# Kernel optimization log

Measured on AMD Instinct MI355X. Metric: run time of the kernel, lower is better.

## Reference

```python
import jax, jax.numpy as jnp
import numpy as np

# Vim-S config
B, L, D, DEPTH = 16, 197, 384, 24
DI, DS, DTR = 768, 16, 24  # d_inner=2*D, d_state, dt_rank=ceil(D/16)
NUM_CLASSES = 1000
EPS = 1e-5


def setup_inputs() -> dict:
    key = jax.random.key(0)
    ks = jax.random.split(key, 12)
    f = jnp.float32
    rn = lambda k, shp, s=0.02: jax.random.normal(k, shp, f) * s
    inp = {
        'x': jax.random.normal(ks[0], (B, 3, 224, 224), f),
        'patch_w': rn(ks[1], (D, 3, 16, 16)),
        'patch_b': jnp.zeros((D,), f),
        'cls_token': rn(ks[2], (1, 1, D)),
        'pos_embed': rn(ks[3], (1, L, D)),
        'in_proj_w': rn(ks[4], (DEPTH, 2 * DI, D)),
        'conv_w': rn(ks[5], (DEPTH, DI, 1, 4), 0.1),  # depthwise causal conv, d_conv=4
        'conv_b': jnp.zeros((DEPTH, DI), f),
        'x_proj_w': rn(ks[6], (DEPTH, DTR + 2 * DS, DI)),
        'dt_proj_w': rn(ks[7], (DEPTH, DI, DTR), 0.1),
        'dt_proj_b': jnp.full((DEPTH, DI), float(np.log(np.expm1(0.01))), f),
        'A_log': jnp.log(jnp.broadcast_to(jnp.arange(1, DS + 1, dtype=f), (DEPTH, DI, DS))),
        'D_ssm': jnp.ones((DEPTH, DI), f),
        'out_proj_w': rn(ks[8], (DEPTH, D, DI)),
        'norm_w': jnp.ones((DEPTH, D), f),
        'norm_b': jnp.zeros((DEPTH, D), f),
        'normf_w': jnp.ones((D,), f),
        'normf_b': jnp.zeros((D,), f),
        'head_w': rn(ks[9], (NUM_CLASSES, D)),
        'head_b': jnp.zeros((NUM_CLASSES,), f),
    }
    return inp


def _ln(u, w, b):
    mu = u.mean(-1, keepdims=True)
    v = ((u - mu) ** 2).mean(-1, keepdims=True)
    return (u - mu) * jax.lax.rsqrt(v + EPS) * w + b


def _silu(u):
    return u * jax.nn.sigmoid(u)


def _mixer(u, Win, Wc, bc, Wx, Wdt, bdt, Alog, Dp, Wout):
    # u: [B, L, D]
    xz = jnp.einsum('bld,ed->ble', u, Win)            # [B, L, 2*DI]
    xc, z = jnp.split(xz, 2, axis=-1)
    # causal depthwise conv1d (d_conv=4): pad 3 on the left
    xt = jnp.pad(xc.transpose(0, 2, 1), ((0, 0), (0, 0), (3, 0)))
    xt = jax.lax.conv_general_dilated(xt, Wc, (1,), 'VALID',
                                      dimension_numbers=('NCH', 'OIH', 'NCH'),
                                      feature_group_count=DI)
    xc = _silu((xt + bc[None, :, None]).transpose(0, 2, 1))  # [B, L, DI]
    dbl = jnp.einsum('bld,ed->ble', xc, Wx)           # [B, L, DTR+2*DS]
    dt = jax.nn.softplus(jnp.einsum('blr,dr->bld', dbl[..., :DTR], Wdt) + bdt)
    Bm = dbl[..., DTR:DTR + DS]                       # [B, L, DS]
    Cm = dbl[..., DTR + DS:]                          # [B, L, DS]
    A = -jnp.exp(Alog)                                # [DI, DS]
    dA = jnp.exp(jnp.einsum('bld,dn->bldn', dt, A))   # [B, L, DI, DS]
    dBx = jnp.einsum('bld,bln->bldn', dt * xc, Bm)    # [B, L, DI, DS]

    def step(h, inps):
        dA_t, dBx_t, C_t = inps
        h = dA_t * h + dBx_t                          # [B, DI, DS]
        return h, jnp.einsum('bdn,bn->bd', h, C_t)

    h0 = jnp.zeros((u.shape[0], DI, DS), u.dtype)
    _, ys = jax.lax.scan(step, h0, (dA.transpose(1, 0, 2, 3),
                                    dBx.transpose(1, 0, 2, 3),
                                    Cm.transpose(1, 0, 2)))
    y = ys.transpose(1, 0, 2) + xc * Dp               # [B, L, DI]
    y = y * _silu(z)
    return jnp.einsum('ble,de->bld', y, Wout)         # [B, L, D]


def reference(x, patch_w, patch_b, cls_token, pos_embed, in_proj_w, conv_w, conv_b,
              x_proj_w, dt_proj_w, dt_proj_b, A_log, D_ssm, out_proj_w,
              norm_w, norm_b, normf_w, normf_b, head_w, head_b):
    b = x.shape[0]
    # patch embed: Conv2d(3, D, 16, stride 16)
    feat = jax.lax.conv_general_dilated(x, patch_w, (16, 16), 'VALID',
                                        dimension_numbers=('NCHW', 'OIHW', 'NCHW'))
    feat = feat + patch_b[None, :, None, None]
    tokens = feat.reshape(b, D, -1).transpose(0, 2, 1)          # [B, 196, D]
    h = jnp.concatenate([jnp.broadcast_to(cls_token, (b, 1, D)), tokens], axis=1)
    h = h + pos_embed                                           # [B, 197, D]

    def layer(carry, p):
        hid, res = carry
        Win, Wc, bc, Wx, Wdt, bdt, Alog, Dp, Wout, nw, nb = p
        res = res + hid                # (hidden + residual), first layer: residual = hidden
        hid = _mixer(_ln(res, nw, nb), Win, Wc, bc, Wx, Wdt, bdt, Alog, Dp, Wout)
        return (hid, res), None

    (hid, res), _ = jax.lax.scan(layer, (h, jnp.zeros_like(h)),
                                 (in_proj_w, conv_w, conv_b, x_proj_w, dt_proj_w,
                                  dt_proj_b, A_log, D_ssm, out_proj_w, norm_w, norm_b))
    out = _ln(res + hid, normf_w, normf_b)
    return out[:, 0] @ head_w.T + head_b                        # [B, num_classes]
```

## Files before the change

kernel.cpp:

```cpp
#include <hip/hip_runtime.h>
#include <hip/hip_bf16.h>
#include <math.h>

#define BB     16
#define LL     197
#define DD     384
#define DEPTH  24
#define DI     768
#define DSN    16
#define DTR    24
#define NC     1000
#define TT     (BB*LL)
#define NPATCH 196
#define EPSV   1e-5f

#define NCHUNK 12
#define CH     17

typedef __attribute__((ext_vector_type(8))) short short8;
typedef __attribute__((ext_vector_type(4))) short short4v;
typedef __attribute__((ext_vector_type(4))) float f32x4;

__device__ __forceinline__ short f2bf(float f) {
  union { float f; unsigned u; } v; v.f = f;
  unsigned u = v.u + 0x7fffu + ((v.u >> 16) & 1u);
  return (short)(u >> 16);
}

__device__ __forceinline__ void gload16(const short* g, const short* l) {
  __builtin_amdgcn_global_load_lds(
      (const __attribute__((address_space(1))) unsigned int*)g,
      (__attribute__((address_space(3))) unsigned int*)l, 16, 0, 0);
}

__global__ __launch_bounds__(256) void k_cvt(const float* __restrict__ src,
                                             short* __restrict__ dst, int n) {
  int i = (blockIdx.x * 256 + threadIdx.x) * 4;
  if (i + 3 < n) {
    float4 v = *(const float4*)&src[i];
    short4v o = {f2bf(v.x), f2bf(v.y), f2bf(v.z), f2bf(v.w)};
    *(short4v*)&dst[i] = o;
  } else {
    for (int j = 0; i + j < n && j < 4; j++) dst[i + j] = f2bf(src[i + j]);
  }
}

__global__ __launch_bounds__(256) void k_init(const float* __restrict__ cls,
                                              const float* __restrict__ pos,
                                              float* __restrict__ res,
                                              float* __restrict__ hid) {
  int i = blockIdx.x * 256 + threadIdx.x;
  if (i < TT * DD) res[i] = 0.f;
  if (i < BB * DD) {
    int b = i / DD, d = i % DD;
    hid[(size_t)(b * LL) * DD + d] = cls[d] + pos[d];
  }
}

__global__ __launch_bounds__(256) void k_patch(const float* __restrict__ x,
                                               const float* __restrict__ pw,
                                               const float* __restrict__ pb,
                                               const float* __restrict__ pos,
                                               float* __restrict__ hid) {
  __shared__ short sA[64 * 40];
  __shared__ short sB[64 * 40];
  const int tid = threadIdx.x;
  const int m0 = blockIdx.x * 64, n0 = blockIdx.y * 64;
  const int srow = tid >> 2;
  const int skq = (tid & 3) * 8;
  const int lane = tid & 63, w = tid >> 6;
  const int wm = (w >> 1) * 32, wn = (w & 1) * 32;
  const int fr = lane & 15;
  const int fk = (lane >> 4) * 8;
  f32x4 acc[2][2] = {};
  const int m = m0 + srow;
  const int b = m / NPATCH;
  const int p = m % NPATCH;
  const int ph = p / 14, pwi = p % 14;
  const float* Wrow = pw + (size_t)(n0 + srow) * 768 + skq;
  for (int k0 = 0; k0 < 768; k0 += 32) {
    int k = k0 + skq;
    int c = k >> 8, rr = (k >> 4) & 15, kw = k & 15;
    const float* xrow = &x[(size_t)(((b * 3 + c) * 224) + (ph * 16 + rr)) * 224 +
                           (pwi * 16 + kw)];
    float4 a0 = *(const float4*)&xrow[0];
    float4 a1 = *(const float4*)&xrow[4];
    float4 b0 = *(const float4*)&Wrow[k0];
    float4 b1 = *(const float4*)&Wrow[k0 + 4];
    short8 av = {f2bf(a0.x), f2bf(a0.y), f2bf(a0.z), f2bf(a0.w),
                 f2bf(a1.x), f2bf(a1.y), f2bf(a1.z), f2bf(a1.w)};
    short8 bv = {f2bf(b0.x), f2bf(b0.y), f2bf(b0.z), f2bf(b0.w),
                 f2bf(b1.x), f2bf(b1.y), f2bf(b1.z), f2bf(b1.w)};
    *(short8*)&sA[srow * 40 + skq] = av;
    *(short8*)&sB[srow * 40 + skq] = bv;
    __syncthreads();
    short8 af0 = *(const short8*)&sA[(wm + fr) * 40 + fk];
    short8 af1 = *(const short8*)&sA[(wm + 16 + fr) * 40 + fk];
    short8 bf0 = *(const short8*)&sB[(wn + fr) * 40 + fk];
    short8 bf1 = *(const short8*)&sB[(wn + 16 + fr) * 40 + fk];
    acc[0][0] = __builtin_amdgcn_mfma_f32_16x16x32_bf16(af0, bf0, acc[0][0], 0, 0, 0);
    acc[0][1] = __builtin_amdgcn_mfma_f32_16x16x32_bf16(af0, bf1, acc[0][1], 0, 0, 0);
    acc[1][0] = __builtin_amdgcn_mfma_f32_16x16x32_bf16(af1, bf0, acc[1][0], 0, 0, 0);
    acc[1][1] = __builtin_amdgcn_mfma_f32_16x16x32_bf16(af1, bf1, acc[1][1], 0, 0, 0);
    __syncthreads();
  }
#pragma unroll
  for (int i = 0; i < 2; i++)
#pragma unroll
    for (int j = 0; j < 2; j++)
#pragma unroll
      for (int q = 0; q < 4; q++) {
        int mm = m0 + wm + i * 16 + (lane >> 4) * 4 + q;
        int nn = n0 + wn + j * 16 + (lane & 15);
        int b2 = mm / NPATCH, pp = mm % NPATCH;
        int tok = b2 * LL + 1 + pp;
        hid[(size_t)tok * DD + nn] = acc[i][j][q] + pb[nn] + pos[(size_t)(1 + pp) * DD + nn];
      }
}

__global__ __launch_bounds__(256) void k_gemm128(const short* __restrict__ A, int lda,
                                                 const short* __restrict__ W, int ldb,
                                                 float* __restrict__ C, int ldc,
                                                 int M, int N, int K) {
  __shared__ short sA[128 * 32];
  __shared__ short sB[128 * 32];
  const int tid = threadIdx.x;
  const int lane = tid & 63, w = tid >> 6;
  const int m0 = blockIdx.x * 128, n0 = blockIdx.y * 128;
  const int wm = (w >> 1) * 64, wn = (w & 1) * 64;
  const int fr = lane & 15;
  const int fk = (lane >> 4) * 8;
  const int q0 = w * 2, q1 = w * 2 + 1;
  const int sr0 = q0 * 16 + (lane >> 2);
  const int sr1 = q1 * 16 + (lane >> 2);
  const int scol = (lane & 3) * 8;
  f32x4 acc[4][4] = {};
  const short* Ab0 = A + (size_t)(m0 + sr0) * lda + scol;
  const short* Ab1 = A + (size_t)(m0 + sr1) * lda + scol;
  const short* Bb0 = W + (size_t)(n0 + sr0) * ldb + scol;
  const short* Bb1 = W + (size_t)(n0 + sr1) * ldb + scol;
  for (int k0 = 0; k0 < K; k0 += 32) {
    gload16(Ab0 + k0, &sA[q0 * 512]);
    gload16(Ab1 + k0, &sA[q1 * 512]);
    gload16(Bb0 + k0, &sB[q0 * 512]);
    gload16(Bb1 + k0, &sB[q1 * 512]);
    __syncthreads();
    short8 af[4], bf[4];
#pragma unroll
    for (int i = 0; i < 4; i++) {
      af[i] = *(const short8*)&sA[(wm + i * 16 + fr) * 32 + fk];
      bf[i] = *(const short8*)&sB[(wn + i * 16 + fr) * 32 + fk];
    }
#pragma unroll
    for (int i = 0; i < 4; i++)
#pragma unroll
      for (int j = 0; j < 4; j++)
        acc[i][j] = __builtin_amdgcn_mfma_f32_16x16x32_bf16(af[i], bf[j], acc[i][j], 0, 0, 0);
    __syncthreads();
  }
#pragma unroll
  for (int i = 0; i < 4; i++)
#pragma unroll
    for (int j = 0; j < 4; j++)
#pragma unroll
      for (int q = 0; q < 4; q++) {
        int mm = m0 + wm + i * 16 + (lane >> 4) * 4 + q;
        int nn = n0 + wn + j * 16 + fr;
        if (mm < M) C[(size_t)mm * ldc + nn] = acc[i][j][q];
      }
}

__global__ __launch_bounds__(256) void k_gemm64(const short* __restrict__ A, int lda,
                                                const short* __restrict__ W, int ldb,
                                                float* __restrict__ C, int ldc,
                                                int M, int N, int K) {
  __shared__ short sA[64 * 32];
  __shared__ short sB[64 * 32];
  const int tid = threadIdx.x;
  const int lane = tid & 63, w = tid >> 6;
  const int m0 = blockIdx.x * 64, n0 = blockIdx.y * 64;
  const int wm = (w >> 1) * 32, wn = (w & 1) * 32;
  const int fr = lane & 15;
  const int fk = (lane >> 4) * 8;
  const int srow = w * 16 + (lane >> 2);
  const int scol = (lane & 3) * 8;
  f32x4 acc[2][2] = {};
  const short* Ab = A + (size_t)(m0 + srow) * lda + scol;
  const short* Bb = W + (size_t)(n0 + srow) * ldb + scol;
  for (int k0 = 0; k0 < K; k0 += 32) {
    gload16(Ab + k0, &sA[w * 512]);
    gload16(Bb + k0, &sB[w * 512]);
    __syncthreads();
    short8 af0 = *(const short8*)&sA[(wm + fr) * 32 + fk];
    short8 af1 = *(const short8*)&sA[(wm + 16 + fr) * 32 + fk];
    short8 bf0 = *(const short8*)&sB[(wn + fr) * 32 + fk];
    short8 bf1 = *(const short8*)&sB[(wn + 16 + fr) * 32 + fk];
    acc[0][0] = __builtin_amdgcn_mfma_f32_16x16x32_bf16(af0, bf0, acc[0][0], 0, 0, 0);
    acc[0][1] = __builtin_amdgcn_mfma_f32_16x16x32_bf16(af0, bf1, acc[0][1], 0, 0, 0);
    acc[1][0] = __builtin_amdgcn_mfma_f32_16x16x32_bf16(af1, bf0, acc[1][0], 0, 0, 0);
    acc[1][1] = __builtin_amdgcn_mfma_f32_16x16x32_bf16(af1, bf1, acc[1][1], 0, 0, 0);
    __syncthreads();
  }
#pragma unroll
  for (int i = 0; i < 2; i++)
#pragma unroll
    for (int j = 0; j < 2; j++)
#pragma unroll
      for (int q = 0; q < 4; q++) {
        int mm = m0 + wm + i * 16 + (lane >> 4) * 4 + q;
        int nn = n0 + wn + j * 16 + fr;
        if (mm < M) C[(size_t)mm * ldc + nn] = acc[i][j][q];
      }
}

__global__ __launch_bounds__(256) void k_dtproj(const float* __restrict__ A,
                                                const short* __restrict__ W,
                                                const float* __restrict__ bias,
                                                float* __restrict__ C) {
  __shared__ short sA[64 * 40];
  __shared__ short sB[64 * 40];
  const int tid = threadIdx.x;
  const int m0 = blockIdx.x * 64, n0 = blockIdx.y * 64;
  const int srow = tid >> 2;
  const int skq = (tid & 3) * 8;
  const int lane = tid & 63, w = tid >> 6;
  const int wm = (w >> 1) * 32, wn = (w & 1) * 32;
  const int fr = lane & 15;
  const int fk = (lane >> 4) * 8;
  f32x4 acc[2][2] = {};
  const int am = m0 + srow;
  short8 av = {0, 0, 0, 0, 0, 0, 0, 0}, bv = {0, 0, 0, 0, 0, 0, 0, 0};
  if (skq < 24) {
    if (am < TT) {
      float4 a0 = *(const float4*)&A[(size_t)am * 56 + skq];
      float4 a1 = *(const float4*)&A[(size_t)am * 56 + skq + 4];
      av = short8{f2bf(a0.x), f2bf(a0.y), f2bf(a0.z), f2bf(a0.w),
                  f2bf(a1.x), f2bf(a1.y), f2bf(a1.z), f2bf(a1.w)};
    }
    bv = *(const short8*)&W[(size_t)(n0 + srow) * 24 + skq];
  }
  *(short8*)&sA[srow * 40 + skq] = av;
  *(short8*)&sB[srow * 40 + skq] = bv;
  __syncthreads();
  short8 af0 = *(const short8*)&sA[(wm + fr) * 40 + fk];
  short8 af1 = *(const short8*)&sA[(wm + 16 + fr) * 40 + fk];
  short8 bf0 = *(const short8*)&sB[(wn + fr) * 40 + fk];
  short8 bf1 = *(const short8*)&sB[(wn + 16 + fr) * 40 + fk];
  acc[0][0] = __builtin_amdgcn_mfma_f32_16x16x32_bf16(af0, bf0, acc[0][0], 0, 0, 0);
  acc[0][1] = __builtin_amdgcn_mfma_f32_16x16x32_bf16(af0, bf1, acc[0][1], 0, 0, 0);
  acc[1][0] = __builtin_amdgcn_mfma_f32_16x16x32_bf16(af1, bf0, acc[1][0], 0, 0, 0);
  acc[1][1] = __builtin_amdgcn_mfma_f32_16x16x32_bf16(af1, bf1, acc[1][1], 0, 0, 0);
#pragma unroll
  for (int i = 0; i < 2; i++)
#pragma unroll
    for (int j = 0; j < 2; j++)
#pragma unroll
      for (int q = 0; q < 4; q++) {
        int mm = m0 + wm + i * 16 + (lane >> 4) * 4 + q;
        int nn = n0 + wn + j * 16 + (lane & 15);
        if (mm < TT) {
          float v = acc[i][j][q] + bias[nn];
          v = (v > 20.f) ? v : log1pf(__expf(v));
          C[(size_t)mm * DI + nn] = v;
        }
      }
}

__global__ __launch_bounds__(256) void k_xproj(const short* __restrict__ A,
                                               const short* __restrict__ W,
                                               float* __restrict__ C) {
  __shared__ short sA[16 * 40];
  __shared__ short sB[64 * 40];
  const int tid = threadIdx.x;
  const int m0 = blockIdx.x * 16;
  const int lane = tid & 63, w = tid >> 6;
  const int wn = w * 16;
  const int fr = lane & 15;
  const int fk = (lane >> 4) * 8;
  const int srow = tid >> 2;
  const int skq = (tid & 3) * 8;
  f32x4 acc = {};
  for (int k0 = 0; k0 < DI; k0 += 32) {
    if (tid < 64) {
      *(short8*)&sA[srow * 40 + skq] =
          *(const short8*)&A[(size_t)(m0 + srow) * DI + k0 + skq];
    }
    short8 bv = {0, 0, 0, 0, 0, 0, 0, 0};
    if (srow < 56) bv = *(const short8*)&W[(size_t)srow * DI + k0 + skq];
    *(short8*)&sB[srow * 40 + skq] = bv;
    __syncthreads();
    short8 af = *(const short8*)&sA[fr * 40 + fk];
    short8 bf = *(const short8*)&sB[(wn + fr) * 40 + fk];
    acc = __builtin_amdgcn_mfma_f32_16x16x32_bf16(af, bf, acc, 0, 0, 0);
    __syncthreads();
  }
#pragma unroll
  for (int q = 0; q < 4; q++) {
    int mm = m0 + (lane >> 4) * 4 + q;
    int nn = wn + (lane & 15);
    if (nn < 56) C[(size_t)mm * 56 + nn] = acc[q];
  }
}

__global__ __launch_bounds__(128) void k_addln(float* __restrict__ res,
                                               const float* __restrict__ hid,
                                               short* __restrict__ u,
                                               const float* __restrict__ nw,
                                               const float* __restrict__ nb) {
  const int t = blockIdx.x;
  const int tid = threadIdx.x;
  float r[3];
  float s = 0.f, sq = 0.f;
#pragma unroll
  for (int j = 0; j < 3; j++) {
    int d = tid + j * 128;
    float v = res[(size_t)t * DD + d] + hid[(size_t)t * DD + d];
    res[(size_t)t * DD + d] = v;
    r[j] = v;
    s += v; sq += v * v;
  }
#pragma unroll
  for (int o = 32; o > 0; o >>= 1) { s += __shfl_xor(s, o); sq += __shfl_xor(sq, o); }
  __shared__ float ls[2], lq[2];
  int w = tid >> 6;
  if ((tid & 63) == 0) { ls[w] = s; lq[w] = sq; }
  __syncthreads();
  float st = ls[0] + ls[1], qt = lq[0] + lq[1];
  float mu = st * (1.f / 384.f);
  float var = qt * (1.f / 384.f) - mu * mu;
  float rs = rsqrtf(var + EPSV);
#pragma unroll
  for (int j = 0; j < 3; j++) {
    int d = tid + j * 128;
    u[(size_t)t * DD + d] = f2bf((r[j] - mu) * rs * nw[d] + nb[d]);
  }
}

__global__ __launch_bounds__(256) void k_conv(const float* __restrict__ xz,
                                              const float* __restrict__ wc,
                                              const float* __restrict__ bc,
                                              float* __restrict__ xc,
                                              short* __restrict__ xcbf) {
  int i = blockIdx.x * 256 + threadIdx.x;
  if (i >= TT * (DI / 4)) return;
  int eg = i % (DI / 4);
  int t = i / (DI / 4);
  int e = eg * 4;
  int b = t / LL, l = t % LL;
  const float* base = xz + (size_t)(b * LL) * (2 * DI) + e;
  float4 w0 = *(const float4*)&wc[(e + 0) * 4];
  float4 w1 = *(const float4*)&wc[(e + 1) * 4];
  float4 w2 = *(const float4*)&wc[(e + 2) * 4];
  float4 w3 = *(const float4*)&wc[(e + 3) * 4];
  float4 acc = *(const float4*)&bc[e];
  if (l >= 3) {
    float4 xv = *(const float4*)&base[(size_t)(l - 3) * (2 * DI)];
    acc.x += xv.x * w0.x; acc.y += xv.y * w1.x; acc.z += xv.z * w2.x; acc.w += xv.w * w3.x;
  }
  if (l >= 2) {
    float4 xv = *(const float4*)&base[(size_t)(l - 2) * (2 * DI)];
    acc.x += xv.x * w0.y; acc.y += xv.y * w1.y; acc.z += xv.z * w2.y; acc.w += xv.w * w3.y;
  }
  if (l >= 1) {
    float4 xv = *(const float4*)&base[(size_t)(l - 1) * (2 * DI)];
    acc.x += xv.x * w0.z; acc.y += xv.y * w1.z; acc.z += xv.z * w2.z; acc.w += xv.w * w3.z;
  }
  {
    float4 xv = *(const float4*)&base[(size_t)l * (2 * DI)];
    acc.x += xv.x * w0.w; acc.y += xv.y * w1.w; acc.z += xv.z * w2.w; acc.w += xv.w * w3.w;
  }
  acc.x = acc.x / (1.f + __expf(-acc.x));
  acc.y = acc.y / (1.f + __expf(-acc.y));
  acc.z = acc.z / (1.f + __expf(-acc.z));
  acc.w = acc.w / (1.f + __expf(-acc.w));
  *(float4*)&xc[(size_t)t * DI + e] = acc;
  short4v ov = {f2bf(acc.x), f2bf(acc.y), f2bf(acc.z), f2bf(acc.w)};
  *(short4v*)&xcbf[(size_t)t * DI + e] = ov;
}

__global__ __launch_bounds__(256) void k_scan1(const float* __restrict__ dt,
                                               const float* __restrict__ xc,
                                               const float* __restrict__ dbl,
                                               const float* __restrict__ Alog,
                                               float* __restrict__ Aprod,
                                               float* __restrict__ Hend) {
  const int tid = threadIdx.x;
  const int e = blockIdx.x * 128 + (tid >> 1);
  const int nh = tid & 1;
  const int b = blockIdx.y;
  const int c = blockIdx.z;
  float4 al0 = *(const float4*)&Alog[(size_t)e * DSN + nh * 8];
  float4 al1 = *(const float4*)&Alog[(size_t)e * DSN + nh * 8 + 4];
  float negA[8] = {-__expf(al0.x), -__expf(al0.y), -__expf(al0.z), -__expf(al0.w),
                   -__expf(al1.x), -__expf(al1.y), -__expf(al1.z), -__expf(al1.w)};
  float h[8] = {};
  float asum = 0.f;
  const int l0 = c * CH;
  const int l1 = (l0 + CH < LL) ? (l0 + CH) : LL;
  const size_t tbase = (size_t)b * LL;
  for (int l = l0; l < l1; l++) {
    size_t t = tbase + l;
    float dtv = dt[t * DI + e];
    float xcv = xc[t * DI + e];
    float4 B0 = *(const float4*)&dbl[t * 56 + DTR + nh * 8];
    float4 B1 = *(const float4*)&dbl[t * 56 + DTR + nh * 8 + 4];
    float dx = dtv * xcv;
    float Bv[8] = {B0.x, B0.y, B0.z, B0.w, B1.x, B1.y, B1.z, B1.w};
#pragma unroll
    for (int j = 0; j < 8; j++)
      h[j] = __expf(dtv * negA[j]) * h[j] + dx * Bv[j];
    asum += dtv;
  }
  size_t ci = (((size_t)c * BB + b) * DI + e) * DSN + nh * 8;
  *(float4*)&Aprod[ci] = float4{__expf(asum * negA[0]), __expf(asum * negA[1]),
                                __expf(asum * negA[2]), __expf(asum * negA[3])};
  *(float4*)&Aprod[ci + 4] = float4{__expf(asum * negA[4]), __expf(asum * negA[5]),
                                    __expf(asum * negA[6]), __expf(asum * negA[7])};
  *(float4*)&Hend[ci] = float4{h[0], h[1], h[2], h[3]};
  *(float4*)&Hend[ci + 4] = float4{h[4], h[5], h[6], h[7]};
}

__global__ __launch_bounds__(256) void k_scan2(const float* __restrict__ dt,
                                               const float* __restrict__ xc,
                                               const float* __restrict__ xz,
                                               const float* __restrict__ dbl,
                                               const float* __restrict__ Alog,
                                               const float* __restrict__ Dp,
                                               const float* __restrict__ Aprod,
                                               const float* __restrict__ Hend,
                                               short* __restrict__ ybf) {
  const int tid = threadIdx.x;
  const int e = blockIdx.x * 128 + (tid >> 1);
  const int nh = tid & 1;
  const int b = blockIdx.y;
  const int c = blockIdx.z;
  float4 al0 = *(const float4*)&Alog[(size_t)e * DSN + nh * 8];
  float4 al1 = *(const float4*)&Alog[(size_t)e * DSN + nh * 8 + 4];
  float negA[8] = {-__expf(al0.x), -__expf(al0.y), -__expf(al0.z), -__expf(al0.w),
                   -__expf(al1.x), -__expf(al1.y), -__expf(al1.z), -__expf(al1.w)};
  const float dpv = Dp[e];
  float h[8] = {};
  const size_t cstride = (size_t)BB * DI * DSN;
  const size_t cbase = (((size_t)b * DI + e) * DSN) + nh * 8;
  for (int cp = 0; cp < c; cp++) {
    size_t ci = (size_t)cp * cstride + cbase;
    float4 a0 = *(const float4*)&Aprod[ci];
    float4 a1 = *(const float4*)&Aprod[ci + 4];
    float4 e0 = *(const float4*)&Hend[ci];
    float4 e1 = *(const float4*)&Hend[ci + 4];
    h[0] = a0.x * h[0] + e0.x; h[1] = a0.y * h[1] + e0.y;
    h[2] = a0.z * h[2] + e0.z; h[3] = a0.w * h[3] + e0.w;
    h[4] = a1.x * h[4] + e1.x; h[5] = a1.y * h[5] + e1.y;
    h[6] = a1.z * h[6] + e1.z; h[7] = a1.w * h[7] + e1.w;
  }
  const int l0 = c * CH;
  const int l1 = (l0 + CH < LL) ? (l0 + CH) : LL;
  const size_t tbase = (size_t)b * LL;
  for (int l = l0; l < l1; l++) {
    size_t t = tbase + l;
    float dtv = dt[t * DI + e];
    float xcv = xc[t * DI + e];
    float zv = xz[t * (2 * DI) + DI + e];
    float4 B0 = *(const float4*)&dbl[t * 56 + DTR + nh * 8];
    float4 B1 = *(const float4*)&dbl[t * 56 + DTR + nh * 8 + 4];
    float4 C0 = *(const float4*)&dbl[t * 56 + DTR + DSN + nh * 8];
    float4 C1 = *(const float4*)&dbl[t * 56 + DTR + DSN + nh * 8 + 4];
    float dx = dtv * xcv;
    float Bv[8] = {B0.x, B0.y, B0.z, B0.w, B1.x, B1.y, B1.z, B1.w};
    float Cv[8] = {C0.x, C0.y, C0.z, C0.w, C1.x, C1.y, C1.z, C1.w};
    float acc = 0.f;
#pragma unroll
    for (int j = 0; j < 8; j++) {
      h[j] = __expf(dtv * negA[j]) * h[j] + dx * Bv[j];
      acc += h[j] * Cv[j];
    }
    acc += __shfl_xor(acc, 1);
    if (nh == 0) {
      float sz = zv * (1.f / (1.f + __expf(-zv)));
      ybf[t * DI + e] = f2bf((acc + xcv * dpv) * sz);
    }
  }
}

__global__ __launch_bounds__(256) void k_final(const float* __restrict__ res,
                                               const float* __restrict__ hid,
                                               const float* __restrict__ nfw,
                                               const float* __restrict__ nfb,
                                               const float* __restrict__ hw,
                                               const float* __restrict__ hb,
                                               float* __restrict__ out) {
  const int b = blockIdx.y;
  const int c0 = blockIdx.x * 125;
  const int tid = threadIdx.x;
  __shared__ float u0[DD];
  __shared__ float ls[4], lq[4];
  const size_t t0 = (size_t)b * LL * DD;
  float v0 = res[t0 + tid] + hid[t0 + tid];
  float v1 = (tid < 128) ? (res[t0 + 256 + tid] + hid[t0 + 256 + tid]) : 0.f;
  float s = v0 + v1, sq = v0 * v0 + v1 * v1;
#pragma unroll
  for (int o = 32; o > 0; o >>= 1) { s += __shfl_xor(s, o); sq += __shfl_xor(sq, o); }
  if ((tid & 63) == 0) { ls[tid >> 6] = s; lq[tid >> 6] = sq; }
  __syncthreads();
  float st = ls[0] + ls[1] + ls[2] + ls[3];
  float qt = lq[0] + lq[1] + lq[2] + lq[3];
  float mu = st * (1.f / 384.f);
  float var = qt * (1.f / 384.f) - mu * mu;
  float rs = rsqrtf(var + EPSV);
  u0[tid] = (v0 - mu) * rs * nfw[tid] + nfb[tid];
  if (tid < 128) u0[256 + tid] = (v1 - mu) * rs * nfw[256 + tid] + nfb[256 + tid];
  __syncthreads();
  int c = c0 + tid;
  if (tid < 125 && c < NC) {
    float acc = hb[c];
    const float* wrow = hw + (size_t)c * DD;
    for (int d = 0; d < DD; d += 4) {
      float4 w4 = *(const float4*)&wrow[d];
      acc += u0[d] * w4.x + u0[d + 1] * w4.y + u0[d + 2] * w4.z + u0[d + 3] * w4.w;
    }
    out[(size_t)b * NC + c] = acc;
  }
}

extern "C" void kernel_launch(void* const* d_in, const int* in_sizes, int n_in,
                              void* d_out, int out_size, void* d_ws, size_t ws_size,
                              hipStream_t stream) {
  const float* x       = (const float*)d_in[0];
  const float* patch_w = (const float*)d_in[1];
  const float* patch_b = (const float*)d_in[2];
  const float* cls     = (const float*)d_in[3];
  const float* pos     = (const float*)d_in[4];
  const float* in_proj = (const float*)d_in[5];
  const float* conv_w  = (const float*)d_in[6];
  const float* conv_b  = (const float*)d_in[7];
  const float* x_proj  = (const float*)d_in[8];
  const float* dt_w    = (const float*)d_in[9];
  const float* dt_b    = (const float*)d_in[10];
  const float* A_log   = (const float*)d_in[11];
  const float* D_ssm   = (const float*)d_in[12];
  const float* out_w   = (const float*)d_in[13];
  const float* norm_w  = (const float*)d_in[14];
  const float* norm_b  = (const float*)d_in[15];
  const float* normf_w = (const float*)d_in[16];
  const float* normf_b = (const float*)d_in[17];
  const float* head_w  = (const float*)d_in[18];
  const float* head_b  = (const float*)d_in[19];
  float* out = (float*)d_out;

  float* ws = (float*)d_ws;
  float* res = ws;  ws += (size_t)TT * DD;
  float* hid = ws;  ws += (size_t)TT * DD;
  float* u_r = ws;  ws += (size_t)TT * DD;
  float* xzb = ws;  ws += (size_t)TT * 2 * DI;
  float* xcb = ws;  ws += (size_t)TT * DI;
  float* dbl = ws;  ws += (size_t)TT * 56;
  float* dtb = ws;  ws += (size_t)TT * DI;
  float* crg = ws;  ws += (size_t)TT * DI;
  float* xcbf_r = ws; ws += (size_t)TT * DI / 2;
  float* ybf_r  = ws; ws += (size_t)TT * DI / 2;
  short* winbf  = (short*)ws; ws += (size_t)DEPTH * 2 * DI * DD / 2;
  short* woutbf = (short*)ws; ws += (size_t)DEPTH * DD * DI / 2;
  short* wxbf   = (short*)ws; ws += (size_t)DEPTH * 56 * DI / 2;
  short* wdtbf  = (short*)ws; ws += (size_t)DEPTH * DI * DTR / 2;

  short* u    = (short*)u_r;
  short* xcbf = (short*)xcbf_r;
  short* ybf  = (short*)ybf_r;
  float* Aprod = crg;
  float* Hend  = hid;

  {
    int n1 = DEPTH * 2 * DI * DD;
    k_cvt<<<(n1 / 4 + 255) / 256, 256, 0, stream>>>(in_proj, winbf, n1);
    int n2 = DEPTH * DD * DI;
    k_cvt<<<(n2 / 4 + 255) / 256, 256, 0, stream>>>(out_w, woutbf, n2);
    int n3 = DEPTH * 56 * DI;
    k_cvt<<<(n3 / 4 + 255) / 256, 256, 0, stream>>>(x_proj, wxbf, n3);
    int n4 = DEPTH * DI * DTR;
    k_cvt<<<(n4 / 4 + 255) / 256, 256, 0, stream>>>(dt_w, wdtbf, n4);
  }

  k_init<<<(TT * DD + 255) / 256, 256, 0, stream>>>(cls, pos, res, hid);
  k_patch<<<dim3(49, 6), 256, 0, stream>>>(x, patch_w, patch_b, pos, hid);

  for (int layer = 0; layer < DEPTH; layer++) {
    k_addln<<<TT, 128, 0, stream>>>(res, hid, u, norm_w + layer * DD, norm_b + layer * DD);
    k_gemm128<<<dim3(25, 12), 256, 0, stream>>>(
        u, DD, winbf + (size_t)layer * 2 * DI * DD, DD, xzb, 2 * DI, TT, 2 * DI, DD);
    k_conv<<<(TT * (DI / 4) + 255) / 256, 256, 0, stream>>>(
        xzb, conv_w + layer * DI * 4, conv_b + layer * DI, xcb, xcbf);
    k_xproj<<<dim3(TT / 16), 256, 0, stream>>>(
        xcbf, wxbf + (size_t)layer * 56 * DI, dbl);
    k_dtproj<<<dim3(50, 12), 256, 0, stream>>>(
        dbl, wdtbf + (size_t)layer * DI * DTR, dt_b + layer * DI, dtb);
    k_scan1<<<dim3(DI / 128, BB, NCHUNK - 1), 256, 0, stream>>>(
        dtb, xcb, dbl, A_log + (size_t)layer * DI * DSN, Aprod, Hend);
    k_scan2<<<dim3(DI / 128, BB, NCHUNK), 256, 0, stream>>>(
        dtb, xcb, xzb, dbl, A_log + (size_t)layer * DI * DSN,
        D_ssm + layer * DI, Aprod, Hend, ybf);
    k_gemm64<<<dim3(50, 6), 256, 0, stream>>>(
        ybf, DI, woutbf + (size_t)layer * DD * DI, DI, hid, DD, TT, DD, DI);
  }

  k_final<<<dim3(8, BB), 256, 0, stream>>>(res, hid, normf_w, normf_b, head_w, head_b, out);
}
```

Baseline: 2.918 ms.

## Fuse conv, x_proj and dt_proj; replace chunked two-pass scan with single-pass scan

New measurement: 5.372 ms. 84.1% more time.

```diff
diff --git a/kernel.cpp b/kernel.cpp
--- a/kernel.cpp
+++ b/kernel.cpp
@@ -13,9 +13,6 @@
 #define TT     (BB*LL)
 #define NPATCH 196
 #define EPSV   1e-5f
-
-#define NCHUNK 12
-#define CH     17
 
 typedef __attribute__((ext_vector_type(8))) short short8;
 typedef __attribute__((ext_vector_type(4))) short short4v;
@@ -213,107 +210,158 @@
       }
 }
 
-__global__ __launch_bounds__(256) void k_dtproj(const float* __restrict__ A,
-                                                const short* __restrict__ W,
-                                                const float* __restrict__ bias,
-                                                float* __restrict__ C) {
-  __shared__ short sA[64 * 40];
-  __shared__ short sB[64 * 40];
-  const int tid = threadIdx.x;
-  const int m0 = blockIdx.x * 64, n0 = blockIdx.y * 64;
-  const int srow = tid >> 2;
-  const int skq = (tid & 3) * 8;
+__global__ __launch_bounds__(256) void k_cxd(const float* __restrict__ xz,
+                                             const float* __restrict__ wc,
+                                             const float* __restrict__ bc,
+                                             const short* __restrict__ wx,
+                                             const short* __restrict__ wdt,
+                                             const float* __restrict__ dbias,
+                                             float* __restrict__ xc,
+                                             float* __restrict__ dbl,
+                                             float* __restrict__ dtb) {
+  __shared__ short sXC[16 * 776];
+  __shared__ short sB[4 * 64 * 32];
+  __shared__ short sDT[16 * 40];
+  const int tid = threadIdx.x;
+  const int t0 = blockIdx.x * 16;
+  for (int it = 0; it < 12; it++) {
+    int g = tid + it * 256;
+    int tl = g / 192, eg = g % 192;
+    int e = eg * 4;
+    int t = t0 + tl;
+    int b = t / LL, l = t % LL;
+    const float* base = xz + (size_t)(b * LL) * (2 * DI) + e;
+    float4 w0 = *(const float4*)&wc[(e + 0) * 4];
+    float4 w1 = *(const float4*)&wc[(e + 1) * 4];
+    float4 w2 = *(const float4*)&wc[(e + 2) * 4];
+    float4 w3 = *(const float4*)&wc[(e + 3) * 4];
+    float4 acc = *(const float4*)&bc[e];
+    if (l >= 3) {
+      float4 xv = *(const float4*)&base[(size_t)(l - 3) * (2 * DI)];
+      acc.x += xv.x * w0.x; acc.y += xv.y * w1.x; acc.z += xv.z * w2.x; acc.w += xv.w * w3.x;
+    }
+    if (l >= 2) {
+      float4 xv = *(const float4*)&base[(size_t)(l - 2) * (2 * DI)];
+      acc.x += xv.x * w0.y; acc.y += xv.y * w1.y; acc.z += xv.z * w2.y; acc.w += xv.w * w3.y;
+    }
+    if (l >= 1) {
+      float4 xv = *(const float4*)&base[(size_t)(l - 1) * (2 * DI)];
+      acc.x += xv.x * w0.z; acc.y += xv.y * w1.z; acc.z += xv.z * w2.z; acc.w += xv.w * w3.z;
+    }
+    {
+      float4 xv = *(const float4*)&base[(size_t)l * (2 * DI)];
+      acc.x += xv.x * w0.w; acc.y += xv.y * w1.w; acc.z += xv.z * w2.w; acc.w += xv.w * w3.w;
+    }
+    acc.x = acc.x / (1.f + __expf(-acc.x));
+    acc.y = acc.y / (1.f + __expf(-acc.y));
+    acc.z = acc.z / (1.f + __expf(-acc.z));
+    acc.w = acc.w / (1.f + __expf(-acc.w));
+    *(float4*)&xc[(size_t)t * DI + e] = acc;
+    short4v ov = {f2bf(acc.x), f2bf(acc.y), f2bf(acc.z), f2bf(acc.w)};
+    *(short4v*)&sXC[tl * 776 + e] = ov;
+  }
+  __syncthreads();
   const int lane = tid & 63, w = tid >> 6;
-  const int wm = (w >> 1) * 32, wn = (w & 1) * 32;
   const int fr = lane & 15;
   const int fk = (lane >> 4) * 8;
-  f32x4 acc[2][2] = {};
-  const int am = m0 + srow;
-  short8 av = {0, 0, 0, 0, 0, 0, 0, 0}, bv = {0, 0, 0, 0, 0, 0, 0, 0};
-  if (skq < 24) {
-    if (am < TT) {
-      float4 a0 = *(const float4*)&A[(size_t)am * 56 + skq];
-      float4 a1 = *(const float4*)&A[(size_t)am * 56 + skq + 4];
-      av = short8{f2bf(a0.x), f2bf(a0.y), f2bf(a0.z), f2bf(a0.w),
-                  f2bf(a1.x), f2bf(a1.y), f2bf(a1.z), f2bf(a1.w)};
-    }
-    bv = *(const short8*)&W[(size_t)(n0 + srow) * 24 + skq];
-  }
-  *(short8*)&sA[srow * 40 + skq] = av;
-  *(short8*)&sB[srow * 40 + skq] = bv;
+  const int srow = w * 16 + (lane >> 2);
+  const int scol = (lane & 3) * 8;
+  const short* Bb = wx + (size_t)srow * DI + scol;
+  f32x4 accx = {};
+  for (int kc = 0; kc < DI; kc += 128) {
+#pragma unroll
+    for (int s = 0; s < 4; s++)
+      gload16(Bb + kc + s * 32, &sB[s * 2048 + w * 512]);
+    __syncthreads();
+#pragma unroll
+    for (int s = 0; s < 4; s++) {
+      short8 af = *(const short8*)&sXC[fr * 776 + kc + s * 32 + fk];
+      short8 bf = *(const short8*)&sB[s * 2048 + (w * 16 + fr) * 32 + fk];
+      accx = __builtin_amdgcn_mfma_f32_16x16x32_bf16(af, bf, accx, 0, 0, 0);
+    }
+    __syncthreads();
+  }
+  {
+    int nn = w * 16 + (lane & 15);
+#pragma unroll
+    for (int q = 0; q < 4; q++) {
+      int row = (lane >> 4) * 4 + q;
+      int t = t0 + row;
+      if (nn >= DTR && nn < 56) dbl[(size_t)t * 56 + nn] = accx[q];
+      if (w < 2) sDT[row * 40 + nn] = (nn < DTR) ? f2bf(accx[q]) : (short)0;
+    }
+  }
   __syncthreads();
-  short8 af0 = *(const short8*)&sA[(wm + fr) * 40 + fk];
-  short8 af1 = *(const short8*)&sA[(wm + 16 + fr) * 40 + fk];
-  short8 bf0 = *(const short8*)&sB[(wn + fr) * 40 + fk];
-  short8 bf1 = *(const short8*)&sB[(wn + 16 + fr) * 40 + fk];
-  acc[0][0] = __builtin_amdgcn_mfma_f32_16x16x32_bf16(af0, bf0, acc[0][0], 0, 0, 0);
-  acc[0][1] = __builtin_amdgcn_mfma_f32_16x16x32_bf16(af0, bf1, acc[0][1], 0, 0, 0);
-  acc[1][0] = __builtin_amdgcn_mfma_f32_16x16x32_bf16(af1, bf0, acc[1][0], 0, 0, 0);
-  acc[1][1] = __builtin_amdgcn_mfma_f32_16x16x32_bf16(af1, bf1, acc[1][1], 0, 0, 0);
-#pragma unroll
-  for (int i = 0; i < 2; i++)
-#pragma unroll
-    for (int j = 0; j < 2; j++)
-#pragma unroll
-      for (int q = 0; q < 4; q++) {
-        int mm = m0 + wm + i * 16 + (lane >> 4) * 4 + q;
-        int nn = n0 + wn + j * 16 + (lane & 15);
-        if (mm < TT) {
-          float v = acc[i][j][q] + bias[nn];
-          v = (v > 20.f) ? v : log1pf(__expf(v));
-          C[(size_t)mm * DI + nn] = v;
-        }
-      }
-}
-
-__global__ __launch_bounds__(256) void k_xproj(const short* __restrict__ A,
-                                               const short* __restrict__ W,
-                                               float* __restrict__ C) {
-  __shared__ short sA[16 * 40];
-  __shared__ short sB[64 * 40];
-  const int tid = threadIdx.x;
-  const int m0 = blockIdx.x * 16;
-  const int lane = tid & 63, w = tid >> 6;
-  const int wn = w * 16;
-  const int fr = lane & 15;
-  const int fk = (lane >> 4) * 8;
-  const int srow = tid >> 2;
-  const int skq = (tid & 3) * 8;
-  f32x4 acc = {};
-  for (int k0 = 0; k0 < DI; k0 += 32) {
-    if (tid < 64) {
-      *(short8*)&sA[srow * 40 + skq] =
-          *(const short8*)&A[(size_t)(m0 + srow) * DI + k0 + skq];
-    }
-    short8 bv = {0, 0, 0, 0, 0, 0, 0, 0};
-    if (srow < 56) bv = *(const short8*)&W[(size_t)srow * DI + k0 + skq];
-    *(short8*)&sB[srow * 40 + skq] = bv;
-    __syncthreads();
-    short8 af = *(const short8*)&sA[fr * 40 + fk];
-    short8 bf = *(const short8*)&sB[(wn + fr) * 40 + fk];
-    acc = __builtin_amdgcn_mfma_f32_16x16x32_bf16(af, bf, acc, 0, 0, 0);
-    __syncthreads();
-  }
-#pragma unroll
-  for (int q = 0; q < 4; q++) {
-    int mm = m0 + (lane >> 4) * 4 + q;
-    int nn = wn + (lane & 15);
-    if (nn < 56) C[(size_t)mm * 56 + nn] = acc[q];
-  }
-}
-
-__global__ __launch_bounds__(128) void k_addln(float* __restrict__ res,
+  short8 adt = *(const short8*)&sDT[fr * 40 + fk];
+  const int g = lane >> 4;
+  for (int jj = 0; jj < 12; jj++) {
+    int j = w * 12 + jj;
+    int row = j * 16 + fr;
+    short8 bdt = {0, 0, 0, 0, 0, 0, 0, 0};
+    if (g < 3) bdt = *(const short8*)&wdt[(size_t)row * DTR + g * 8];
+    f32x4 p = {};
+    p = __builtin_amdgcn_mfma_f32_16x16x32_bf16(adt, bdt, p, 0, 0, 0);
+    int nn = j * 16 + (lane & 15);
+    float bv = dbias[nn];
+#pragma unroll
+    for (int q = 0; q < 4; q++) {
+      int t = t0 + (lane >> 4) * 4 + q;
+      float v = p[q] + bv;
+      v = (v > 20.f) ? v : log1pf(__expf(v));
+      dtb[(size_t)t * DI + nn] = v;
+    }
+  }
+}
+
+__global__ __launch_bounds__(256) void k_scan(const float* __restrict__ dt,
+                                              const float* __restrict__ xc,
+                                              const float* __restrict__ xz,
+                                              const float* __restrict__ dbl,
+                                              const float* __restrict__ Alog,
+                                              const float* __restrict__ Dp,
+                                              short* __restrict__ ybf) {
+  const int tid = threadIdx.x;
+  const int e = blockIdx.x * 32 + (tid >> 3);
+  const int nh = tid & 7;
+  const int b = blockIdx.y;
+  float2 al = *(const float2*)&Alog[(size_t)e * DSN + nh * 2];
+  const float negA0 = -__expf(al.x), negA1 = -__expf(al.y);
+  const float dpv = Dp[e];
+  float h0 = 0.f, h1 = 0.f;
+  const size_t tbase = (size_t)b * LL;
+  for (int l = 0; l < LL; l++) {
+    size_t t = tbase + l;
+    float dtv = dt[t * DI + e];
+    float xcv = xc[t * DI + e];
+    float zv = xz[t * (2 * DI) + DI + e];
+    float2 Bv = *(const float2*)&dbl[t * 56 + DTR + nh * 2];
+    float2 Cv = *(const float2*)&dbl[t * 56 + DTR + DSN + nh * 2];
+    float dx = dtv * xcv;
+    h0 = __expf(dtv * negA0) * h0 + dx * Bv.x;
+    h1 = __expf(dtv * negA1) * h1 + dx * Bv.y;
+    float acc = h0 * Cv.x + h1 * Cv.y;
+    acc += __shfl_xor(acc, 1);
+    acc += __shfl_xor(acc, 2);
+    acc += __shfl_xor(acc, 4);
+    if (nh == 0) {
+      float sz = zv * (1.f / (1.f + __expf(-zv)));
+      ybf[t * DI + e] = f2bf((acc + xcv * dpv) * sz);
+    }
+  }
+}
+
+__global__ __launch_bounds__(256) void k_addln(float* __restrict__ res,
                                                const float* __restrict__ hid,
                                                short* __restrict__ u,
                                                const float* __restrict__ nw,
                                                const float* __restrict__ nb) {
-  const int t = blockIdx.x;
-  const int tid = threadIdx.x;
-  float r[3];
+  const int lane = threadIdx.x & 63;
+  const int t = blockIdx.x * 4 + (threadIdx.x >> 6);
+  float r[6];
   float s = 0.f, sq = 0.f;
 #pragma unroll
-  for (int j = 0; j < 3; j++) {
-    int d = tid + j * 128;
+  for (int j = 0; j < 6; j++) {
+    int d = lane + j * 64;
     float v = res[(size_t)t * DD + d] + hid[(size_t)t * DD + d];
     res[(size_t)t * DD + d] = v;
     r[j] = v;
@@ -321,164 +369,13 @@
   }
 #pragma unroll
   for (int o = 32; o > 0; o >>= 1) { s += __shfl_xor(s, o); sq += __shfl_xor(sq, o); }
-  __shared__ float ls[2], lq[2];
-  int w = tid >> 6;
-  if ((tid & 63) == 0) { ls[w] = s; lq[w] = sq; }
-  __syncthreads();
-  float st = ls[0] + ls[1], qt = lq[0] + lq[1];
-  float mu = st * (1.f / 384.f);
-  float var = qt * (1.f / 384.f) - mu * mu;
+  float mu = s * (1.f / 384.f);
+  float var = sq * (1.f / 384.f) - mu * mu;
   float rs = rsqrtf(var + EPSV);
 #pragma unroll
-  for (int j = 0; j < 3; j++) {
-    int d = tid + j * 128;
+  for (int j = 0; j < 6; j++) {
+    int d = lane + j * 64;
     u[(size_t)t * DD + d] = f2bf((r[j] - mu) * rs * nw[d] + nb[d]);
-  }
-}
-
-__global__ __launch_bounds__(256) void k_conv(const float* __restrict__ xz,
-                                              const float* __restrict__ wc,
-                                              const float* __restrict__ bc,
-                                              float* __restrict__ xc,
-                                              short* __restrict__ xcbf) {
-  int i = blockIdx.x * 256 + threadIdx.x;
-  if (i >= TT * (DI / 4)) return;
-  int eg = i % (DI / 4);
-  int t = i / (DI / 4);
-  int e = eg * 4;
-  int b = t / LL, l = t % LL;
-  const float* base = xz + (size_t)(b * LL) * (2 * DI) + e;
-  float4 w0 = *(const float4*)&wc[(e + 0) * 4];
-  float4 w1 = *(const float4*)&wc[(e + 1) * 4];
-  float4 w2 = *(const float4*)&wc[(e + 2) * 4];
-  float4 w3 = *(const float4*)&wc[(e + 3) * 4];
-  float4 acc = *(const float4*)&bc[e];
-  if (l >= 3) {
-    float4 xv = *(const float4*)&base[(size_t)(l - 3) * (2 * DI)];
-    acc.x += xv.x * w0.x; acc.y += xv.y * w1.x; acc.z += xv.z * w2.x; acc.w += xv.w * w3.x;
-  }
-  if (l >= 2) {
-    float4 xv = *(const float4*)&base[(size_t)(l - 2) * (2 * DI)];
-    acc.x += xv.x * w0.y; acc.y += xv.y * w1.y; acc.z += xv.z * w2.y; acc.w += xv.w * w3.y;
-  }
-  if (l >= 1) {
-    float4 xv = *(const float4*)&base[(size_t)(l - 1) * (2 * DI)];
-    acc.x += xv.x * w0.z; acc.y += xv.y * w1.z; acc.z += xv.z * w2.z; acc.w += xv.w * w3.z;
-  }
-  {
-    float4 xv = *(const float4*)&base[(size_t)l * (2 * DI)];
-    acc.x += xv.x * w0.w; acc.y += xv.y * w1.w; acc.z += xv.z * w2.w; acc.w += xv.w * w3.w;
-  }
-  acc.x = acc.x / (1.f + __expf(-acc.x));
-  acc.y = acc.y / (1.f + __expf(-acc.y));
-  acc.z = acc.z / (1.f + __expf(-acc.z));
-  acc.w = acc.w / (1.f + __expf(-acc.w));
-  *(float4*)&xc[(size_t)t * DI + e] = acc;
-  short4v ov = {f2bf(acc.x), f2bf(acc.y), f2bf(acc.z), f2bf(acc.w)};
-  *(short4v*)&xcbf[(size_t)t * DI + e] = ov;
-}
-
-__global__ __launch_bounds__(256) void k_scan1(const float* __restrict__ dt,
-                                               const float* __restrict__ xc,
-                                               const float* __restrict__ dbl,
-                                               const float* __restrict__ Alog,
-                                               float* __restrict__ Aprod,
-                                               float* __restrict__ Hend) {
-  const int tid = threadIdx.x;
-  const int e = blockIdx.x * 128 + (tid >> 1);
-  const int nh = tid & 1;
-  const int b = blockIdx.y;
-  const int c = blockIdx.z;
-  float4 al0 = *(const float4*)&Alog[(size_t)e * DSN + nh * 8];
-  float4 al1 = *(const float4*)&Alog[(size_t)e * DSN + nh * 8 + 4];
-  float negA[8] = {-__expf(al0.x), -__expf(al0.y), -__expf(al0.z), -__expf(al0.w),
-                   -__expf(al1.x), -__expf(al1.y), -__expf(al1.z), -__expf(al1.w)};
-  float h[8] = {};
-  float asum = 0.f;
-  const int l0 = c * CH;
-  const int l1 = (l0 + CH < LL) ? (l0 + CH) : LL;
-  const size_t tbase = (size_t)b * LL;
-  for (int l = l0; l < l1; l++) {
-    size_t t = tbase + l;
-    float dtv = dt[t * DI + e];
-    float xcv = xc[t * DI + e];
-    float4 B0 = *(const float4*)&dbl[t * 56 + DTR + nh * 8];
-    float4 B1 = *(const float4*)&dbl[t * 56 + DTR + nh * 8 + 4];
-    float dx = dtv * xcv;
-    float Bv[8] = {B0.x, B0.y, B0.z, B0.w, B1.x, B1.y, B1.z, B1.w};
-#pragma unroll
-    for (int j = 0; j < 8; j++)
-      h[j] = __expf(dtv * negA[j]) * h[j] + dx * Bv[j];
-    asum += dtv;
-  }
-  size_t ci = (((size_t)c * BB + b) * DI + e) * DSN + nh * 8;
-  *(float4*)&Aprod[ci] = float4{__expf(asum * negA[0]), __expf(asum * negA[1]),
-                                __expf(asum * negA[2]), __expf(asum * negA[3])};
-  *(float4*)&Aprod[ci + 4] = float4{__expf(asum * negA[4]), __expf(asum * negA[5]),
-                                    __expf(asum * negA[6]), __expf(asum * negA[7])};
-  *(float4*)&Hend[ci] = float4{h[0], h[1], h[2], h[3]};
-  *(float4*)&Hend[ci + 4] = float4{h[4], h[5], h[6], h[7]};
-}
-
-__global__ __launch_bounds__(256) void k_scan2(const float* __restrict__ dt,
-                                               const float* __restrict__ xc,
-                                               const float* __restrict__ xz,
-                                               const float* __restrict__ dbl,
-                                               const float* __restrict__ Alog,
-                                               const float* __restrict__ Dp,
-                                               const float* __restrict__ Aprod,
-                                               const float* __restrict__ Hend,
-                                               short* __restrict__ ybf) {
-  const int tid = threadIdx.x;
-  const int e = blockIdx.x * 128 + (tid >> 1);
-  const int nh = tid & 1;
-  const int b = blockIdx.y;
-  const int c = blockIdx.z;
-  float4 al0 = *(const float4*)&Alog[(size_t)e * DSN + nh * 8];
-  float4 al1 = *(const float4*)&Alog[(size_t)e * DSN + nh * 8 + 4];
-  float negA[8] = {-__expf(al0.x), -__expf(al0.y), -__expf(al0.z), -__expf(al0.w),
-                   -__expf(al1.x), -__expf(al1.y), -__expf(al1.z), -__expf(al1.w)};
-  const float dpv = Dp[e];
-  float h[8] = {};
-  const size_t cstride = (size_t)BB * DI * DSN;
-  const size_t cbase = (((size_t)b * DI + e) * DSN) + nh * 8;
-  for (int cp = 0; cp < c; cp++) {
-    size_t ci = (size_t)cp * cstride + cbase;
-    float4 a0 = *(const float4*)&Aprod[ci];
-    float4 a1 = *(const float4*)&Aprod[ci + 4];
-    float4 e0 = *(const float4*)&Hend[ci];
-    float4 e1 = *(const float4*)&Hend[ci + 4];
-    h[0] = a0.x * h[0] + e0.x; h[1] = a0.y * h[1] + e0.y;
-    h[2] = a0.z * h[2] + e0.z; h[3] = a0.w * h[3] + e0.w;
-    h[4] = a1.x * h[4] + e1.x; h[5] = a1.y * h[5] + e1.y;
-    h[6] = a1.z * h[6] + e1.z; h[7] = a1.w * h[7] + e1.w;
-  }
-  const int l0 = c * CH;
-  const int l1 = (l0 + CH < LL) ? (l0 + CH) : LL;
-  const size_t tbase = (size_t)b * LL;
-  for (int l = l0; l < l1; l++) {
-    size_t t = tbase + l;
-    float dtv = dt[t * DI + e];
-    float xcv = xc[t * DI + e];
-    float zv = xz[t * (2 * DI) + DI + e];
-    float4 B0 = *(const float4*)&dbl[t * 56 + DTR + nh * 8];
-    float4 B1 = *(const float4*)&dbl[t * 56 + DTR + nh * 8 + 4];
-    float4 C0 = *(const float4*)&dbl[t * 56 + DTR + DSN + nh * 8];
-    float4 C1 = *(const float4*)&dbl[t * 56 + DTR + DSN + nh * 8 + 4];
-    float dx = dtv * xcv;
-    float Bv[8] = {B0.x, B0.y, B0.z, B0.w, B1.x, B1.y, B1.z, B1.w};
-    float Cv[8] = {C0.x, C0.y, C0.z, C0.w, C1.x, C1.y, C1.z, C1.w};
-    float acc = 0.f;
-#pragma unroll
-    for (int j = 0; j < 8; j++) {
-      h[j] = __expf(dtv * negA[j]) * h[j] + dx * Bv[j];
-      acc += h[j] * Cv[j];
-    }
-    acc += __shfl_xor(acc, 1);
-    if (nh == 0) {
-      float sz = zv * (1.f / (1.f + __expf(-zv)));
-      ybf[t * DI + e] = f2bf((acc + xcv * dpv) * sz);
-    }
   }
 }
 
@@ -555,19 +452,14 @@
   float* xcb = ws;  ws += (size_t)TT * DI;
   float* dbl = ws;  ws += (size_t)TT * 56;
   float* dtb = ws;  ws += (size_t)TT * DI;
-  float* crg = ws;  ws += (size_t)TT * DI;
-  float* xcbf_r = ws; ws += (size_t)TT * DI / 2;
-  float* ybf_r  = ws; ws += (size_t)TT * DI / 2;
+  float* ybf_r = ws; ws += (size_t)TT * DI / 2;
   short* winbf  = (short*)ws; ws += (size_t)DEPTH * 2 * DI * DD / 2;
   short* woutbf = (short*)ws; ws += (size_t)DEPTH * DD * DI / 2;
   short* wxbf   = (short*)ws; ws += (size_t)DEPTH * 56 * DI / 2;
   short* wdtbf  = (short*)ws; ws += (size_t)DEPTH * DI * DTR / 2;
 
   short* u    = (short*)u_r;
-  short* xcbf = (short*)xcbf_r;
   short* ybf  = (short*)ybf_r;
-  float* Aprod = crg;
-  float* Hend  = hid;
 
   {
     int n1 = DEPTH * 2 * DI * DD;
@@ -584,20 +476,17 @@
   k_patch<<<dim3(49, 6), 256, 0, stream>>>(x, patch_w, patch_b, pos, hid);
 
   for (int layer = 0; layer < DEPTH; layer++) {
-    k_addln<<<TT, 128, 0, stream>>>(res, hid, u, norm_w + layer * DD, norm_b + layer * DD);
+    k_addln<<<TT / 4, 256, 0, stream>>>(res, hid, u, norm_w + layer * DD,
+                                        norm_b + layer * DD);
     k_gemm128<<<dim3(25, 12), 256, 0, stream>>>(
         u, DD, winbf + (size_t)layer * 2 * DI * DD, DD, xzb, 2 * DI, TT, 2 * DI, DD);
-    k_conv<<<(TT * (DI / 4) + 255) / 256, 256, 0, stream>>>(
-        xzb, conv_w + layer * DI * 4, conv_b + layer * DI, xcb, xcbf);
-    k_xproj<<<dim3(TT / 16), 256, 0, stream>>>(
-        xcbf, wxbf + (size_t)layer * 56 * DI, dbl);
-    k_dtproj<<<dim3(50, 12), 256, 0, stream>>>(
-        dbl, wdtbf + (size_t)layer * DI * DTR, dt_b + layer * DI, dtb);
-    k_scan1<<<dim3(DI / 128, BB, NCHUNK - 1), 256, 0, stream>>>(
-        dtb, xcb, dbl, A_log + (size_t)layer * DI * DSN, Aprod, Hend);
-    k_scan2<<<dim3(DI / 128, BB, NCHUNK), 256, 0, stream>>>(
+    k_cxd<<<dim3(TT / 16), 256, 0, stream>>>(
+        xzb, conv_w + layer * DI * 4, conv_b + layer * DI,
+        wxbf + (size_t)layer * 56 * DI, wdtbf + (size_t)layer * DI * DTR,
+        dt_b + layer * DI, xcb, dbl, dtb);
+    k_scan<<<dim3(DI / 32, BB), 256, 0, stream>>>(
         dtb, xcb, xzb, dbl, A_log + (size_t)layer * DI * DSN,
-        D_ssm + layer * DI, Aprod, Hend, ybf);
+        D_ssm + layer * DI, ybf);
     k_gemm64<<<dim3(50, 6), 256, 0, stream>>>(
         ybf, DI, woutbf + (size_t)layer * DD * DI, DI, hid, DD, TT, DD, DI);
   }
```
